# Kernel tuning notes

Hardware: AMD Instinct MI355X
Metric: run time of the kernel (lower is better)

Reference implementation:

```python
import jax, jax.numpy as jnp
import numpy as np

HID = 256
NUM_ENT = 100000
NUM_REL = 50
E = 320000  # edges per direction; edge_index has 2*E columns
BN_EPS = 1e-5


def setup_inputs() -> dict:
    key = jax.random.key(0)
    ks = jax.random.split(key, 10)
    x = jax.random.normal(ks[0], (NUM_ENT, HID), dtype=jnp.float32)
    edge_index = jax.random.randint(ks[1], (2, 2 * E), 0, NUM_ENT)
    edge_type = jax.random.randint(ks[2], (2 * E,), 0, NUM_REL)
    rel_embed = jax.random.normal(ks[3], (NUM_REL, HID), dtype=jnp.float32)
    # xavier_normal init: std = sqrt(2 / (fan_in + fan_out))
    w_std = (2.0 / (HID + HID)) ** 0.5
    w_loop = jax.random.normal(ks[4], (HID, HID), dtype=jnp.float32) * w_std
    w_in = jax.random.normal(ks[5], (HID, HID), dtype=jnp.float32) * w_std
    w_out = jax.random.normal(ks[6], (HID, HID), dtype=jnp.float32) * w_std
    w_rel = jax.random.normal(ks[7], (HID, HID), dtype=jnp.float32) * w_std
    loop_rel = jax.random.normal(ks[8], (1, HID), dtype=jnp.float32) * ((2.0 / (1 + HID)) ** 0.5)
    bn_weight = jnp.ones((HID,), dtype=jnp.float32)
    bn_bias = jnp.zeros((HID,), dtype=jnp.float32)
    return {
        "x": x, "edge_index": edge_index, "edge_type": edge_type,
        "rel_embed": rel_embed, "w_loop": w_loop, "w_in": w_in,
        "w_out": w_out, "w_rel": w_rel, "loop_rel": loop_rel,
        "bn_weight": bn_weight, "bn_bias": bn_bias,
    }


def _compute_norm(edge_index, num_ent):
    # symmetric D^-1/2 * D^-1/2 norm; degree counted on row (target) index
    row, col = edge_index[0], edge_index[1]
    deg = jax.ops.segment_sum(jnp.ones_like(row, dtype=jnp.float32), row, num_segments=num_ent)
    deg_inv = jnp.where(deg > 0, deg ** -0.5, 0.0)
    return deg_inv[row] * deg_inv[col]


def _propagate(x, idx, etype, rel_all, W, norm, num_ent):
    # gather source nodes (idx[1]), compose with relation emb (mult), transform, scale, scatter-add to targets (idx[0])
    msg = (x[idx[1]] * rel_all[etype]) @ W  # [E, d]
    if norm is not None:
        msg = msg * norm[:, None]
    return jax.ops.segment_sum(msg, idx[0], num_segments=num_ent)


def reference(x, edge_index, edge_type, rel_embed, w_loop, w_in, w_out, w_rel,
              loop_rel, bn_weight, bn_bias):
    num_ent = x.shape[0]
    rel_all = jnp.concatenate([rel_embed, loop_rel], axis=0)  # [R+1, d]
    e = edge_index.shape[1] // 2
    in_index, out_index = edge_index[:, :e], edge_index[:, e:]
    in_type, out_type = edge_type[:e], edge_type[e:]

    in_norm = _compute_norm(in_index, num_ent)
    out_norm = _compute_norm(out_index, num_ent)

    in_res = _propagate(x, in_index, in_type, rel_all, w_in, in_norm, num_ent)
    out_res = _propagate(x, out_index, out_type, rel_all, w_out, out_norm, num_ent)
    # self-loop: identity scatter -> just per-node compose+transform
    loop_res = (x * loop_rel) @ w_loop

    out = (in_res + out_res + loop_res) * (1.0 / 3.0)

    # BatchNorm1d in training mode (batch stats, biased variance)
    mean = out.mean(axis=0)
    var = out.var(axis=0)
    out = (out - mean) * jax.lax.rsqrt(var + BN_EPS) * bn_weight + bn_bias

    rel_out = (rel_all @ w_rel)[:-1]  # drop loop relation
    return out, rel_out
```

## Files before the change

### kernel.cpp

```cpp
#include <hip/hip_runtime.h>

#define HID     256
#define N_ENT   100000
#define TOT_E   640000
#define HALF_E  320000
#define NSEG    (2 * N_ENT)
#define BN_EPSF 1e-5f
#define SCAN_ELEMS 1024
#define NBLK_SCAN  ((NSEG + SCAN_ELEMS - 1) / SCAN_ELEMS)

typedef short bf16x8 __attribute__((ext_vector_type(8)));
typedef short bf16x4 __attribute__((ext_vector_type(4)));
typedef float f32x4  __attribute__((ext_vector_type(4)));

__device__ __forceinline__ short f2b(float f) {
    union { float f; unsigned u; } c; c.f = f;
    unsigned u = c.u;
    u += 0x7FFF + ((u >> 16) & 1);
    return (short)(u >> 16);
}
__device__ __forceinline__ float b2f(short b) {
    union { unsigned u; float f; } c;
    c.u = ((unsigned)(unsigned short)b) << 16;
    return c.f;
}

__global__ void hist_kernel(const int* __restrict__ ei, int* __restrict__ offs) {
    int j = blockIdx.x * 256 + threadIdx.x;
    if (j >= TOT_E) return;
    int seg = ei[j] + ((j < HALF_E) ? 0 : N_ENT);
    atomicAdd(&offs[seg], 1);
}

__global__ __launch_bounds__(256) void scan1(int* __restrict__ offs, int* __restrict__ bsums,
                                             float* __restrict__ rnorm) {
    __shared__ int tsum[256];
    int b = blockIdx.x, t = threadIdx.x;
    int base = b * SCAN_ELEMS + t * 4;
    int v[4] = {0, 0, 0, 0};
    if (base + 3 < NSEG) {
        int4 lv = *(const int4*)(offs + base);
        v[0] = lv.x; v[1] = lv.y; v[2] = lv.z; v[3] = lv.w;
    } else {
        for (int i = 0; i < 4; ++i) if (base + i < NSEG) v[i] = offs[base + i];
    }
    #pragma unroll
    for (int i = 0; i < 4; ++i)
        if (base + i < NSEG)
            rnorm[base + i] = (v[i] > 0) ? rsqrtf((float)v[i]) : 0.f;
    tsum[t] = v[0] + v[1] + v[2] + v[3];
    __syncthreads();
    for (int d = 1; d < 256; d <<= 1) {
        int val = (t >= d) ? tsum[t - d] : 0;
        __syncthreads();
        tsum[t] += val;
        __syncthreads();
    }
    int run = (t == 0) ? 0 : tsum[t - 1];
    if (t == 255) bsums[b] = tsum[255];
    int w[4];
    for (int i = 0; i < 4; ++i) { w[i] = run; run += v[i]; }
    if (base + 3 < NSEG) *(int4*)(offs + base) = make_int4(w[0], w[1], w[2], w[3]);
    else for (int i = 0; i < 4; ++i) if (base + i < NSEG) offs[base + i] = w[i];
}

__global__ __launch_bounds__(256) void scan3f(int* __restrict__ offs, const int* __restrict__ bsums) {
    __shared__ int tmp[256];
    int b = blockIdx.x, t = threadIdx.x;
    tmp[t] = (t < NBLK_SCAN) ? bsums[t] : 0;
    __syncthreads();
    for (int d = 1; d < 256; d <<= 1) {
        int val = (t >= d) ? tmp[t - d] : 0;
        __syncthreads();
        tmp[t] += val;
        __syncthreads();
    }
    int add = (b == 0) ? 0 : tmp[b - 1];
    int base = b * SCAN_ELEMS + t * 4;
    if (base + 3 < NSEG) {
        int4 v = *(int4*)(offs + base);
        v.x += add; v.y += add; v.z += add; v.w += add;
        *(int4*)(offs + base) = v;
    } else {
        for (int i = 0; i < 4; ++i) if (base + i < NSEG) offs[base + i] += add;
    }
}

__global__ void fill8_kernel(const int* __restrict__ ei, const int* __restrict__ et,
                             int* __restrict__ offs, const float* __restrict__ rnorm,
                             int2* __restrict__ elist8) {
    int j = blockIdx.x * 256 + threadIdx.x;
    if (j >= TOT_E) return;
    int hb  = (j < HALF_E) ? 0 : N_ENT;
    int seg = ei[j] + hb;
    int col = ei[TOT_E + j];
    float norm = rnorm[seg] * rnorm[hb + col];
    int pos = atomicAdd(&offs[seg], 1);
    elist8[pos] = make_int2(col | (et[j] << 17), __float_as_int(norm));
}

#define NX8 (N_ENT * HID / 8)
#define NR8 (50 * HID / 8)
__global__ void tobf16_both(const float* __restrict__ x, short* __restrict__ xh,
                            const float* __restrict__ rel, short* __restrict__ relh) {
    int i = blockIdx.x * 256 + threadIdx.x;
    const float* src; short* dst; int idx;
    if (i < NX8) { src = x; dst = xh; idx = i; }
    else if (i < NX8 + NR8) { src = rel; dst = relh; idx = i - NX8; }
    else return;
    const float4* p = (const float4*)(src + (size_t)idx * 8);
    float4 v0 = p[0], v1 = p[1];
    bf16x8 pk;
    pk[0]=f2b(v0.x); pk[1]=f2b(v0.y); pk[2]=f2b(v0.z); pk[3]=f2b(v0.w);
    pk[4]=f2b(v1.x); pk[5]=f2b(v1.y); pk[6]=f2b(v1.z); pk[7]=f2b(v1.w);
    *(bf16x8*)(dst + (size_t)idx * 8) = pk;
}

__global__ __launch_bounds__(256) void gather_h(
        const short* __restrict__ xh, const short* __restrict__ relh,
        const int* __restrict__ offs, const int2* __restrict__ elist8,
        short* __restrict__ accA, short* __restrict__ accB) {
    int s = blockIdx.x * 4 + (threadIdx.x >> 6);
    int lane = threadIdx.x & 63;
    int start = (s == 0) ? 0 : offs[s - 1];
    int end   = offs[s];
    float ax0=0.f, ay0=0.f, az0=0.f, aw0=0.f;
    float ax1=0.f, ay1=0.f, az1=0.f, aw1=0.f;
    int e = start;
    for (; e + 2 <= end; e += 2) {
        int2 p0 = elist8[e];
        int2 p1 = elist8[e + 1];
        int   c0 = p0.x & 0x1FFFF, t0 = p0.x >> 17;
        float n0 = __int_as_float(p0.y);
        int   c1 = p1.x & 0x1FFFF, t1 = p1.x >> 17;
        float n1 = __int_as_float(p1.y);
        bf16x4 xv0 = *(const bf16x4*)(xh   + (size_t)c0 * HID + lane * 4);
        bf16x4 rv0 = *(const bf16x4*)(relh + (size_t)t0 * HID + lane * 4);
        bf16x4 xv1 = *(const bf16x4*)(xh   + (size_t)c1 * HID + lane * 4);
        bf16x4 rv1 = *(const bf16x4*)(relh + (size_t)t1 * HID + lane * 4);
        ax0 += b2f(xv0[0]) * b2f(rv0[0]) * n0;
        ay0 += b2f(xv0[1]) * b2f(rv0[1]) * n0;
        az0 += b2f(xv0[2]) * b2f(rv0[2]) * n0;
        aw0 += b2f(xv0[3]) * b2f(rv0[3]) * n0;
        ax1 += b2f(xv1[0]) * b2f(rv1[0]) * n1;
        ay1 += b2f(xv1[1]) * b2f(rv1[1]) * n1;
        az1 += b2f(xv1[2]) * b2f(rv1[2]) * n1;
        aw1 += b2f(xv1[3]) * b2f(rv1[3]) * n1;
    }
    if (e < end) {
        int2 p = elist8[e];
        int   c = p.x & 0x1FFFF, t = p.x >> 17;
        float n = __int_as_float(p.y);
        bf16x4 xv = *(const bf16x4*)(xh   + (size_t)c * HID + lane * 4);
        bf16x4 rv = *(const bf16x4*)(relh + (size_t)t * HID + lane * 4);
        ax0 += b2f(xv[0]) * b2f(rv[0]) * n;
        ay0 += b2f(xv[1]) * b2f(rv[1]) * n;
        az0 += b2f(xv[2]) * b2f(rv[2]) * n;
        aw0 += b2f(xv[3]) * b2f(rv[3]) * n;
    }
    int hb = (s >= N_ENT) ? N_ENT : 0;
    short* dst = ((s >= N_ENT) ? accB : accA) + (size_t)(s - hb) * HID + lane * 4;
    bf16x4 pk;
    pk[0] = f2b(ax0 + ax1); pk[1] = f2b(ay0 + ay1);
    pk[2] = f2b(az0 + az1); pk[3] = f2b(aw0 + aw1);
    *(bf16x4*)dst = pk;
}

__global__ void wcat_kernel(const float* __restrict__ w_in, const float* __restrict__ w_out,
                            const float* __restrict__ w_loop, const float* __restrict__ loop_rel,
                            short* __restrict__ WT) {
    int n = blockIdx.x;
    int t = threadIdx.x;
    float v0 = w_in  [(size_t)t * HID + n];
    float v1 = w_out [(size_t)t * HID + n];
    float v2 = w_loop[(size_t)t * HID + n] * loop_rel[t];
    short* row = WT + (size_t)n * 768;
    row[t]       = f2b(v0);
    row[256 + t] = f2b(v1);
    row[512 + t] = f2b(v2);
}

template <bool BF16OUT>
__global__ __launch_bounds__(256, 2) void gemm_mfma_128(
        const short* __restrict__ accA, const short* __restrict__ accB,
        const short* __restrict__ xh, const short* __restrict__ WT,
        float* __restrict__ out, short* __restrict__ outh, float* __restrict__ stats)
{
    __shared__ __align__(16) short As[128 * 64];
    __shared__ __align__(16) short Bs[256 * 64];
    const int tid = threadIdx.x;
    const int l   = tid & 63;
    const int wid = tid >> 6;
    const int r0  = blockIdx.x * 128;
    const int lr  = l & 15;
    const int lg  = l >> 4;

    f32x4 acc[8][4];
    #pragma unroll
    for (int i = 0; i < 8; ++i)
        #pragma unroll
        for (int j = 0; j < 4; ++j)
            acc[i][j] = (f32x4){0.f, 0.f, 0.f, 0.f};

    const int sg = tid & 7;
    const int sr = tid >> 3;

    for (int kt = 0; kt < 12; ++kt) {
        const int src = kt >> 2;
        const short* Ap = (src == 0) ? accA : ((src == 1) ? accB : xh);
        const int ksg = kt * 64;
        const int ksl = (kt & 3) * 64;
        __syncthreads();
        #pragma unroll
        for (int h = 0; h < 4; ++h) {
            int r  = sr + 32 * h;
            int gr = r0 + r;
            bf16x8 v = {0,0,0,0,0,0,0,0};
            if (gr < N_ENT) v = *(const bf16x8*)(Ap + (size_t)gr * HID + ksl + sg * 8);
            *(bf16x8*)&As[r * 64 + ((sg ^ (r & 7)) << 3)] = v;
        }
        #pragma unroll
        for (int i = 0; i < 8; ++i) {
            int n = sr + 32 * i;
            bf16x8 w = *(const bf16x8*)(WT + (size_t)n * 768 + ksg + sg * 8);
            *(bf16x8*)&Bs[n * 64 + ((sg ^ (n & 7)) << 3)] = w;
        }
        __syncthreads();
        #pragma unroll
        for (int kc = 0; kc < 2; ++kc) {
            const int gsel = kc * 4 + lg;
            bf16x8 bfr[4];
            #pragma unroll
            for (int j = 0; j < 4; ++j) {
                int n = wid * 64 + 16 * j + lr;
                bfr[j] = *(const bf16x8*)&Bs[n * 64 + ((gsel ^ (n & 7)) << 3)];
            }
            #pragma unroll
            for (int i = 0; i < 8; ++i) {
                int r = 16 * i + lr;
                bf16x8 af = *(const bf16x8*)&As[r * 64 + ((gsel ^ (r & 7)) << 3)];
                #pragma unroll
                for (int j = 0; j < 4; ++j)
                    acc[i][j] = __builtin_amdgcn_mfma_f32_16x16x32_bf16(
                                    af, bfr[j], acc[i][j], 0, 0, 0);
            }
        }
    }

    const float third = 1.f / 3.f;
    float s[4]  = {0.f, 0.f, 0.f, 0.f};
    float sq[4] = {0.f, 0.f, 0.f, 0.f};
    #pragma unroll
    for (int i = 0; i < 8; ++i) {
        #pragma unroll
        for (int v = 0; v < 4; ++v) {
            int grow = r0 + 16 * i + lg * 4 + v;
            if (grow < N_ENT) {
                #pragma unroll
                for (int j = 0; j < 4; ++j) {
                    float val = acc[i][j][v] * third;
                    int col = wid * 64 + 16 * j + lr;
                    if (BF16OUT) outh[(size_t)grow * HID + col] = f2b(val);
                    else         out [(size_t)grow * HID + col] = val;
                    s[j] += val; sq[j] += val * val;
                }
            }
        }
    }
    #pragma unroll
    for (int j = 0; j < 4; ++j) {
        s[j]  += __shfl_xor(s[j], 16);  s[j]  += __shfl_xor(s[j], 32);
        sq[j] += __shfl_xor(sq[j], 16); sq[j] += __shfl_xor(sq[j], 32);
    }
    if (lg == 0) {
        #pragma unroll
        for (int j = 0; j < 4; ++j) {
            int c = wid * 64 + 16 * j + lr;
            atomicAdd(&stats[c], s[j]);
            atomicAdd(&stats[HID + c], sq[j]);
        }
    }
}

__global__ void bn_apply_h(const short* __restrict__ outh, float* __restrict__ out,
                           const float* __restrict__ stats,
                           const float* __restrict__ bnw, const float* __restrict__ bnb) {
    const float invN = 1.f / (float)N_ENT;
    const int total8 = N_ENT * (HID / 8);
    for (int i = blockIdx.x * 256 + threadIdx.x; i < total8; i += gridDim.x * 256) {
        int c = (i & 31) * 8;
        bf16x8 v = *(const bf16x8*)(outh + (size_t)i * 8);
        float r[8];
        #pragma unroll
        for (int k = 0; k < 8; ++k) {
            float mean = stats[c + k] * invN;
            float var  = stats[HID + c + k] * invN - mean * mean;
            float sc   = rsqrtf(var + BN_EPSF) * bnw[c + k];
            float sh   = bnb[c + k] - mean * sc;
            r[k] = b2f(v[k]) * sc + sh;
        }
        float4* dst = (float4*)(out + (size_t)i * 8);
        dst[0] = make_float4(r[0], r[1], r[2], r[3]);
        dst[1] = make_float4(r[4], r[5], r[6], r[7]);
    }
}

__global__ void bn_apply(float* __restrict__ out, const float* __restrict__ stats,
                         const float* __restrict__ bnw, const float* __restrict__ bnb) {
    const float invN = 1.f / (float)N_ENT;
    const int total4 = N_ENT * (HID / 4);
    for (int i = blockIdx.x * 256 + threadIdx.x; i < total4; i += gridDim.x * 256) {
        int c = (i & 63) * 4;
        float4 v = *(float4*)(out + (size_t)i * 4);
        #pragma unroll
        for (int k = 0; k < 4; ++k) {
            float mean = stats[c + k] * invN;
            float var  = stats[HID + c + k] * invN - mean * mean;
            float sc   = rsqrtf(var + BN_EPSF) * bnw[c + k];
            float sh   = bnb[c + k] - mean * sc;
            float* comp = (k == 0) ? &v.x : (k == 1) ? &v.y : (k == 2) ? &v.z : &v.w;
            *comp = (*comp) * sc + sh;
        }
        *(float4*)(out + (size_t)i * 4) = v;
    }
}

__global__ void relout_kernel(const float* __restrict__ rel_embed,
                              const float* __restrict__ w_rel,
                              float* __restrict__ rel_out) {
    __shared__ float row[HID];
    int r = blockIdx.x;
    int c = threadIdx.x;
    row[c] = rel_embed[(size_t)r * HID + c];
    __syncthreads();
    float s = 0.f;
    #pragma unroll 8
    for (int k = 0; k < HID; ++k) s += row[k] * w_rel[(size_t)k * HID + c];
    rel_out[(size_t)r * HID + c] = s;
}

extern "C" void kernel_launch(void* const* d_in, const int* in_sizes, int n_in,
                              void* d_out, int out_size, void* d_ws, size_t ws_size,
                              hipStream_t stream) {
    const float* x        = (const float*)d_in[0];
    const int*   ei       = (const int*)d_in[1];
    const int*   et       = (const int*)d_in[2];
    const float* rel      = (const float*)d_in[3];
    const float* w_loop   = (const float*)d_in[4];
    const float* w_in     = (const float*)d_in[5];
    const float* w_out    = (const float*)d_in[6];
    const float* w_rel    = (const float*)d_in[7];
    const float* loop_rel = (const float*)d_in[8];
    const float* bnw      = (const float*)d_in[9];
    const float* bnb      = (const float*)d_in[10];

    float* out     = (float*)d_out;
    float* rel_out = out + (size_t)N_ENT * HID;

    const size_t XH_B   = (size_t)N_ENT * HID * 2;
    const size_t ACC_B  = (size_t)N_ENT * HID * 2;
    const size_t OFFS_B = (size_t)NSEG * 4;
    const size_t EL8_B  = (size_t)TOT_E * 8;
    const size_t RN_B   = (size_t)NSEG * 4;
    const size_t RELH_B = (size_t)50 * HID * 2;
    const size_t base_need = XH_B + 2 * ACC_B + OFFS_B + EL8_B + RN_B
                           + 256 * 4 + 512 * 4 + RELH_B;
    const size_t OUTH_B = (size_t)N_ENT * HID * 2;
    const bool   have_outh = (ws_size >= base_need + OUTH_B);

    char* w = (char*)d_ws;
    short* xh     = (short*)w;              w += XH_B;
    short* accA_h = (short*)w;              w += ACC_B;
    short* accB_h = (short*)w;              w += ACC_B;
    int*   offs   = (int*)w;                w += OFFS_B;
    int2*  elist8 = (int2*)w;               short* WT = (short*)w;   w += EL8_B;
    float* rnorm  = (float*)w;              w += RN_B;
    int*   bsums  = (int*)w;                w += 256 * 4;
    float* stats  = (float*)w;              w += 512 * 4;
    short* relh   = (short*)w;              w += RELH_B;
    short* outh   = (short*)w;

    hipMemsetAsync(offs, 0, OFFS_B, stream);
    hipMemsetAsync(stats, 0, 512 * 4, stream);

    tobf16_both<<<(NX8 + NR8 + 255) / 256, 256, 0, stream>>>(x, xh, rel, relh);
    hist_kernel<<<TOT_E / 256, 256, 0, stream>>>(ei, offs);
    scan1<<<NBLK_SCAN, 256, 0, stream>>>(offs, bsums, rnorm);
    scan3f<<<NBLK_SCAN, 256, 0, stream>>>(offs, bsums);
    fill8_kernel<<<TOT_E / 256, 256, 0, stream>>>(ei, et, offs, rnorm, elist8);
    gather_h<<<NSEG / 4, 256, 0, stream>>>(xh, relh, offs, elist8, accA_h, accB_h);
    wcat_kernel<<<256, 256, 0, stream>>>(w_in, w_out, w_loop, loop_rel, WT);
    if (have_outh) {
        gemm_mfma_128<true><<<(N_ENT + 127) / 128, 256, 0, stream>>>(
            accA_h, accB_h, xh, WT, out, outh, stats);
        bn_apply_h<<<1024, 256, 0, stream>>>(outh, out, stats, bnw, bnb);
    } else {
        gemm_mfma_128<false><<<(N_ENT + 127) / 128, 256, 0, stream>>>(
            accA_h, accB_h, xh, WT, out, outh, stats);
        bn_apply<<<1024, 256, 0, stream>>>(out, stats, bnw, bnb);
    }
    relout_kernel<<<50, 256, 0, stream>>>(rel, w_rel, rel_out);
}
```

Before: 321.7 us.

## Load GEMM fragments directly from global and fuse small prep/epilogue kernels

Replaces the LDS-staged MFMA GEMM with a version where each wave loads bf16 fragments straight from global memory into registers and computes a 64x128 tile, removing shared-memory staging and barriers. It also merges the memsets, bf16 conversion and weight concat into one prep kernel, and folds the relation projection into the BN apply kernel, to cut launch overhead. WT gets a dedicated workspace slot. Risks: strided, poorly coalesced global fragment loads and heavier reliance on caches for reuse.

```diff
diff --git a/kernel.cpp b/kernel.cpp
--- a/kernel.cpp
+++ b/kernel.cpp
@@ -23,6 +23,44 @@
     union { unsigned u; float f; } c;
     c.u = ((unsigned)(unsigned short)b) << 16;
     return c.f;
+}
+
+#define NX8 (N_ENT * HID / 8)
+#define NR8 (50 * HID / 8)
+#define CONV_BLOCKS ((NX8 + NR8 + 255) / 256)
+__global__ void prep_kernel(const float* __restrict__ x, short* __restrict__ xh,
+                            const float* __restrict__ rel, short* __restrict__ relh,
+                            const float* __restrict__ w_in, const float* __restrict__ w_out,
+                            const float* __restrict__ w_loop, const float* __restrict__ loop_rel,
+                            short* __restrict__ WT,
+                            int* __restrict__ offs, float* __restrict__ stats) {
+    int bid = blockIdx.x;
+    int tid = threadIdx.x;
+    if (bid < CONV_BLOCKS) {
+        int i = bid * 256 + tid;
+        if (i < NSEG) offs[i] = 0;
+        if (i < 512) stats[i] = 0.f;
+        const float* src; short* dst; int idx;
+        if (i < NX8) { src = x; dst = xh; idx = i; }
+        else if (i < NX8 + NR8) { src = rel; dst = relh; idx = i - NX8; }
+        else return;
+        const float4* p = (const float4*)(src + (size_t)idx * 8);
+        float4 v0 = p[0], v1 = p[1];
+        bf16x8 pk;
+        pk[0]=f2b(v0.x); pk[1]=f2b(v0.y); pk[2]=f2b(v0.z); pk[3]=f2b(v0.w);
+        pk[4]=f2b(v1.x); pk[5]=f2b(v1.y); pk[6]=f2b(v1.z); pk[7]=f2b(v1.w);
+        *(bf16x8*)(dst + (size_t)idx * 8) = pk;
+    } else {
+        int n = bid - CONV_BLOCKS;
+        int t = tid;
+        float v0 = w_in  [(size_t)t * HID + n];
+        float v1 = w_out [(size_t)t * HID + n];
+        float v2 = w_loop[(size_t)t * HID + n] * loop_rel[t];
+        short* row = WT + (size_t)n * 768;
+        row[t]       = f2b(v0);
+        row[256 + t] = f2b(v1);
+        row[512 + t] = f2b(v2);
+    }
 }
 
 __global__ void hist_kernel(const int* __restrict__ ei, int* __restrict__ offs) {
@@ -97,23 +135,6 @@
     float norm = rnorm[seg] * rnorm[hb + col];
     int pos = atomicAdd(&offs[seg], 1);
     elist8[pos] = make_int2(col | (et[j] << 17), __float_as_int(norm));
-}
-
-#define NX8 (N_ENT * HID / 8)
-#define NR8 (50 * HID / 8)
-__global__ void tobf16_both(const float* __restrict__ x, short* __restrict__ xh,
-                            const float* __restrict__ rel, short* __restrict__ relh) {
-    int i = blockIdx.x * 256 + threadIdx.x;
-    const float* src; short* dst; int idx;
-    if (i < NX8) { src = x; dst = xh; idx = i; }
-    else if (i < NX8 + NR8) { src = rel; dst = relh; idx = i - NX8; }
-    else return;
-    const float4* p = (const float4*)(src + (size_t)idx * 8);
-    float4 v0 = p[0], v1 = p[1];
-    bf16x8 pk;
-    pk[0]=f2b(v0.x); pk[1]=f2b(v0.y); pk[2]=f2b(v0.z); pk[3]=f2b(v0.w);
-    pk[4]=f2b(v1.x); pk[5]=f2b(v1.y); pk[6]=f2b(v1.z); pk[7]=f2b(v1.w);
-    *(bf16x8*)(dst + (size_t)idx * 8) = pk;
 }
 
 __global__ __launch_bounds__(256) void gather_h(
@@ -166,100 +187,79 @@
     *(bf16x4*)dst = pk;
 }
 
-__global__ void wcat_kernel(const float* __restrict__ w_in, const float* __restrict__ w_out,
-                            const float* __restrict__ w_loop, const float* __restrict__ loop_rel,
-                            short* __restrict__ WT) {
-    int n = blockIdx.x;
-    int t = threadIdx.x;
-    float v0 = w_in  [(size_t)t * HID + n];
-    float v1 = w_out [(size_t)t * HID + n];
-    float v2 = w_loop[(size_t)t * HID + n] * loop_rel[t];
-    short* row = WT + (size_t)n * 768;
-    row[t]       = f2b(v0);
-    row[256 + t] = f2b(v1);
-    row[512 + t] = f2b(v2);
-}
-
 template <bool BF16OUT>
-__global__ __launch_bounds__(256, 2) void gemm_mfma_128(
+__global__ __launch_bounds__(256) void gemm_direct(
         const short* __restrict__ accA, const short* __restrict__ accB,
         const short* __restrict__ xh, const short* __restrict__ WT,
         float* __restrict__ out, short* __restrict__ outh, float* __restrict__ stats)
 {
-    __shared__ __align__(16) short As[128 * 64];
-    __shared__ __align__(16) short Bs[256 * 64];
     const int tid = threadIdx.x;
     const int l   = tid & 63;
     const int wid = tid >> 6;
-    const int r0  = blockIdx.x * 128;
+    const int wr  = wid >> 1;
+    const int wc  = wid & 1;
+    const int r0  = blockIdx.x * 128 + wr * 64;
+    const int c0  = wc * 128;
     const int lr  = l & 15;
     const int lg  = l >> 4;
-
-    f32x4 acc[8][4];
-    #pragma unroll
-    for (int i = 0; i < 8; ++i)
+    const int lgo = lg * 8;
+
+    f32x4 acc[4][8];
+    #pragma unroll
+    for (int i = 0; i < 4; ++i)
         #pragma unroll
-        for (int j = 0; j < 4; ++j)
+        for (int j = 0; j < 8; ++j)
             acc[i][j] = (f32x4){0.f, 0.f, 0.f, 0.f};
 
-    const int sg = tid & 7;
-    const int sr = tid >> 3;
-
-    for (int kt = 0; kt < 12; ++kt) {
-        const int src = kt >> 2;
-        const short* Ap = (src == 0) ? accA : ((src == 1) ? accB : xh);
-        const int ksg = kt * 64;
-        const int ksl = (kt & 3) * 64;
-        __syncthreads();
-        #pragma unroll
-        for (int h = 0; h < 4; ++h) {
-            int r  = sr + 32 * h;
-            int gr = r0 + r;
-            bf16x8 v = {0,0,0,0,0,0,0,0};
-            if (gr < N_ENT) v = *(const bf16x8*)(Ap + (size_t)gr * HID + ksl + sg * 8);
-            *(bf16x8*)&As[r * 64 + ((sg ^ (r & 7)) << 3)] = v;
+    int rowoff[4];
+    #pragma unroll
+    for (int i = 0; i < 4; ++i) {
+        int gr = r0 + 16 * i + lr;
+        if (gr >= N_ENT) gr = N_ENT - 1;
+        rowoff[i] = gr * HID;
+    }
+    int coloff[8];
+    #pragma unroll
+    for (int j = 0; j < 8; ++j)
+        coloff[j] = (c0 + 16 * j + lr) * 768;
+
+    #pragma unroll 1
+    for (int src = 0; src < 3; ++src) {
+        const short* __restrict__ Ap = (src == 0) ? accA : ((src == 1) ? accB : xh);
+        #pragma unroll 2
+        for (int c8 = 0; c8 < 8; ++c8) {
+            const int ka = c8 * 32 + lgo;
+            const int kb = src * 256 + c8 * 32 + lgo;
+            bf16x8 af[4], bfr[8];
+            #pragma unroll
+            for (int i = 0; i < 4; ++i)
+                af[i] = *(const bf16x8*)(Ap + (size_t)(rowoff[i] + ka));
+            #pragma unroll
+            for (int j = 0; j < 8; ++j)
+                bfr[j] = *(const bf16x8*)(WT + (size_t)(coloff[j] + kb));
+            #pragma unroll
+            for (int j = 0; j < 8; ++j)
+                #pragma unroll
+                for (int i = 0; i < 4; ++i)
+                    acc[i][j] = __builtin_amdgcn_mfma_f32_16x16x32_bf16(
+                                    af[i], bfr[j], acc[i][j], 0, 0, 0);
         }
-        #pragma unroll
-        for (int i = 0; i < 8; ++i) {
-            int n = sr + 32 * i;
-            bf16x8 w = *(const bf16x8*)(WT + (size_t)n * 768 + ksg + sg * 8);
-            *(bf16x8*)&Bs[n * 64 + ((sg ^ (n & 7)) << 3)] = w;
-        }
-        __syncthreads();
-        #pragma unroll
-        for (int kc = 0; kc < 2; ++kc) {
-            const int gsel = kc * 4 + lg;
-            bf16x8 bfr[4];
-            #pragma unroll
-            for (int j = 0; j < 4; ++j) {
-                int n = wid * 64 + 16 * j + lr;
-                bfr[j] = *(const bf16x8*)&Bs[n * 64 + ((gsel ^ (n & 7)) << 3)];
-            }
-            #pragma unroll
-            for (int i = 0; i < 8; ++i) {
-                int r = 16 * i + lr;
-                bf16x8 af = *(const bf16x8*)&As[r * 64 + ((gsel ^ (r & 7)) << 3)];
-                #pragma unroll
-                for (int j = 0; j < 4; ++j)
-                    acc[i][j] = __builtin_amdgcn_mfma_f32_16x16x32_bf16(
-                                    af, bfr[j], acc[i][j], 0, 0, 0);
-            }
-        }
     }
 
     const float third = 1.f / 3.f;
-    float s[4]  = {0.f, 0.f, 0.f, 0.f};
-    float sq[4] = {0.f, 0.f, 0.f, 0.f};
-    #pragma unroll
-    for (int i = 0; i < 8; ++i) {
+    float s[8], sq[8];
+    #pragma unroll
+    for (int j = 0; j < 8; ++j) { s[j] = 0.f; sq[j] = 0.f; }
+    #pragma unroll
+    for (int i = 0; i < 4; ++i) {
         #pragma unroll
         for (int v = 0; v < 4; ++v) {
             int grow = r0 + 16 * i + lg * 4 + v;
             if (grow < N_ENT) {
                 #pragma unroll
-                for (int j = 0; j < 4; ++j) {
+                for (int j = 0; j < 8; ++j) {
                     float val = acc[i][j][v] * third;
-                    int col = wid * 64 + 16 * j + lr;
+                    int col = c0 + 16 * j + lr;
                     if (BF16OUT) outh[(size_t)grow * HID + col] = f2b(val);
                     else         out [(size_t)grow * HID + col] = val;
                     s[j] += val; sq[j] += val * val;
@@ -268,75 +268,90 @@
         }
     }
     #pragma unroll
-    for (int j = 0; j < 4; ++j) {
+    for (int j = 0; j < 8; ++j) {
         s[j]  += __shfl_xor(s[j], 16);  s[j]  += __shfl_xor(s[j], 32);
         sq[j] += __shfl_xor(sq[j], 16); sq[j] += __shfl_xor(sq[j], 32);
     }
     if (lg == 0) {
         #pragma unroll
-        for (int j = 0; j < 4; ++j) {
-            int c = wid * 64 + 16 * j + lr;
+        for (int j = 0; j < 8; ++j) {
+            int c = c0 + 16 * j + lr;
             atomicAdd(&stats[c], s[j]);
             atomicAdd(&stats[HID + c], sq[j]);
         }
     }
 }
 
-__global__ void bn_apply_h(const short* __restrict__ outh, float* __restrict__ out,
-                           const float* __restrict__ stats,
-                           const float* __restrict__ bnw, const float* __restrict__ bnb) {
-    const float invN = 1.f / (float)N_ENT;
-    const int total8 = N_ENT * (HID / 8);
-    for (int i = blockIdx.x * 256 + threadIdx.x; i < total8; i += gridDim.x * 256) {
-        int c = (i & 31) * 8;
-        bf16x8 v = *(const bf16x8*)(outh + (size_t)i * 8);
-        float r[8];
-        #pragma unroll
-        for (int k = 0; k < 8; ++k) {
-            float mean = stats[c + k] * invN;
-            float var  = stats[HID + c + k] * invN - mean * mean;
-            float sc   = rsqrtf(var + BN_EPSF) * bnw[c + k];
-            float sh   = bnb[c + k] - mean * sc;
-            r[k] = b2f(v[k]) * sc + sh;
+#define BN_BLOCKS 1024
+__global__ void bn_relout_h(const short* __restrict__ outh, float* __restrict__ out,
+                            const float* __restrict__ stats,
+                            const float* __restrict__ bnw, const float* __restrict__ bnb,
+                            const float* __restrict__ rel_embed, const float* __restrict__ w_rel,
+                            float* __restrict__ rel_out) {
+    if (blockIdx.x < BN_BLOCKS) {
+        const float invN = 1.f / (float)N_ENT;
+        const int total8 = N_ENT * (HID / 8);
+        for (int i = blockIdx.x * 256 + threadIdx.x; i < total8; i += BN_BLOCKS * 256) {
+            int c = (i & 31) * 8;
+            bf16x8 v = *(const bf16x8*)(outh + (size_t)i * 8);
+            float r[8];
+            #pragma unroll
+            for (int k = 0; k < 8; ++k) {
+                float mean = stats[c + k] * invN;
+                float var  = stats[HID + c + k] * invN - mean * mean;
+                float sc   = rsqrtf(var + BN_EPSF) * bnw[c + k];
+                float sh   = bnb[c + k] - mean * sc;
+                r[k] = b2f(v[k]) * sc + sh;
+            }
+            float4* dst = (float4*)(out + (size_t)i * 8);
+            dst[0] = make_float4(r[0], r[1], r[2], r[3]);
+            dst[1] = make_float4(r[4], r[5], r[6], r[7]);
         }
-        float4* dst = (float4*)(out + (size_t)i * 8);
-        dst[0] = make_float4(r[0], r[1], r[2], r[3]);
-        dst[1] = make_float4(r[4], r[5], r[6], r[7]);
-    }
-}
-
-__global__ void bn_apply(float* __restrict__ out, const float* __restrict__ stats,
-                         const float* __restrict__ bnw, const float* __restrict__ bnb) {
-    const float invN = 1.f / (float)N_ENT;
-    const int total4 = N_ENT * (HID / 4);
-    for (int i = blockIdx.x * 256 + threadIdx.x; i < total4; i += gridDim.x * 256) {
-        int c = (i & 63) * 4;
-        float4 v = *(float4*)(out + (size_t)i * 4);
-        #pragma unroll
-        for (int k = 0; k < 4; ++k) {
-            float mean = stats[c + k] * invN;
-            float var  = stats[HID + c + k] * invN - mean * mean;
-            float sc   = rsqrtf(var + BN_EPSF) * bnw[c + k];
-            float sh   = bnb[c + k] - mean * sc;
-            float* comp = (k == 0) ? &v.x : (k == 1) ? &v.y : (k == 2) ? &v.z : &v.w;
-            *comp = (*comp) * sc + sh;
+    } else {
+        __shared__ float row[HID];
+        int r = blockIdx.x - BN_BLOCKS;
+        int c = threadIdx.x;
+        row[c] = rel_embed[(size_t)r * HID + c];
+        __syncthreads();
+        float sum = 0.f;
+        #pragma unroll 8
+        for (int k = 0; k < HID; ++k) sum += row[k] * w_rel[(size_t)k * HID + c];
+        rel_out[(size_t)r * HID + c] = sum;
+    }
+}
+
+__global__ void bn_relout_f(float* __restrict__ out, const float* __restrict__ stats,
+                            const float* __restrict__ bnw, const float* __restrict__ bnb,
+                            const float* __restrict__ rel_embed, const float* __restrict__ w_rel,
+                            float* __restrict__ rel_out) {
+    if (blockIdx.x < BN_BLOCKS) {
+        const float invN = 1.f / (float)N_ENT;
+        const int total4 = N_ENT * (HID / 4);
+        for (int i = blockIdx.x * 256 + threadIdx.x; i < total4; i += BN_BLOCKS * 256) {
+            int c = (i & 63) * 4;
+            float4 v = *(float4*)(out + (size_t)i * 4);
+            #pragma unroll
+            for (int k = 0; k < 4; ++k) {
+                float mean = stats[c + k] * invN;
+                float var  = stats[HID + c + k] * invN - mean * mean;
+                float sc   = rsqrtf(var + BN_EPSF) * bnw[c + k];
+                float sh   = bnb[c + k] - mean * sc;
+                float* comp = (k == 0) ? &v.x : (k == 1) ? &v.y : (k == 2) ? &v.z : &v.w;
+                *comp = (*comp) * sc + sh;
+            }
+            *(float4*)(out + (size_t)i * 4) = v;
         }
-        *(float4*)(out + (size_t)i * 4) = v;
-    }
-}
-
-__global__ void relout_kernel(const float* __restrict__ rel_embed,
-                              const float* __restrict__ w_rel,
-                              float* __restrict__ rel_out) {
-    __shared__ float row[HID];
-    int r = blockIdx.x;
-    int c = threadIdx.x;
-    row[c] = rel_embed[(size_t)r * HID + c];
-    __syncthreads();
-    float s = 0.f;
-    #pragma unroll 8
-    for (int k = 0; k < HID; ++k) s += row[k] * w_rel[(size_t)k * HID + c];
-    rel_out[(size_t)r * HID + c] = s;
+    } else {
+        __shared__ float row[HID];
+        int r = blockIdx.x - BN_BLOCKS;
+        int c = threadIdx.x;
+        row[c] = rel_embed[(size_t)r * HID + c];
+        __syncthreads();
+        float sum = 0.f;
+        #pragma unroll 8
+        for (int k = 0; k < HID; ++k) sum += row[k] * w_rel[(size_t)k * HID + c];
+        rel_out[(size_t)r * HID + c] = sum;
+    }
 }
 
 extern "C" void kernel_launch(void* const* d_in, const int* in_sizes, int n_in,
@@ -363,8 +378,9 @@
     const size_t EL8_B  = (size_t)TOT_E * 8;
     const size_t RN_B   = (size_t)NSEG * 4;
     const size_t RELH_B = (size_t)50 * HID * 2;
+    const size_t WT_B   = (size_t)256 * 768 * 2;
     const size_t base_need = XH_B + 2 * ACC_B + OFFS_B + EL8_B + RN_B
-                           + 256 * 4 + 512 * 4 + RELH_B;
+                           + 256 * 4 + 512 * 4 + RELH_B + WT_B;
     const size_t OUTH_B = (size_t)N_ENT * HID * 2;
     const bool   have_outh = (ws_size >= base_need + OUTH_B);
 
@@ -373,31 +389,31 @@
     short* accA_h = (short*)w;              w += ACC_B;
     short* accB_h = (short*)w;              w += ACC_B;
     int*   offs   = (int*)w;                w += OFFS_B;
-    int2*  elist8 = (int2*)w;               short* WT = (short*)w;   w += EL8_B;
+    int2*  elist8 = (int2*)w;               w += EL8_B;
     float* rnorm  = (float*)w;              w += RN_B;
     int*   bsums  = (int*)w;                w += 256 * 4;
     float* stats  = (float*)w;              w += 512 * 4;
     short* relh   = (short*)w;              w += RELH_B;
+    short* WT     = (short*)w;              w += WT_B;
     short* outh   = (short*)w;
 
-    hipMemsetAsync(offs, 0, OFFS_B, stream);
-    hipMemsetAsync(stats, 0, 512 * 4, stream);
-
-    tobf16_both<<<(NX8 + NR8 + 255) / 256, 256, 0, stream>>>(x, xh, rel, relh);
+    prep_kernel<<<CONV_BLOCKS + 256, 256, 0, stream>>>(x, xh, rel, relh,
+                                                       w_in, w_out, w_loop, loop_rel,
+                                                       WT, offs, stats);
     hist_kernel<<<TOT_E / 256, 256, 0, stream>>>(ei, offs);
     scan1<<<NBLK_SCAN, 256, 0, stream>>>(offs, bsums, rnorm);
     scan3f<<<NBLK_SCAN, 256, 0, stream>>>(offs, bsums);
     fill8_kernel<<<TOT_E / 256, 256, 0, stream>>>(ei, et, offs, rnorm, elist8);
     gather_h<<<NSEG / 4, 256, 0, stream>>>(xh, relh, offs, elist8, accA_h, accB_h);
-    wcat_kernel<<<256, 256, 0, stream>>>(w_in, w_out, w_loop, loop_rel, WT);
     if (have_outh) {
-        gemm_mfma_128<true><<<(N_ENT + 127) / 128, 256, 0, stream>>>(
+        gemm_direct<true><<<(N_ENT + 127) / 128, 256, 0, stream>>>(
             accA_h, accB_h, xh, WT, out, outh, stats);
-        bn_apply_h<<<1024, 256, 0, stream>>>(outh, out, stats, bnw, bnb);
-    } else {
-        gemm_mfma_128<false><<<(N_ENT + 127) / 128, 256, 0, stream>>>(
+        bn_relout_h<<<BN_BLOCKS + 50, 256, 0, stream>>>(outh, out, stats, bnw, bnb,
+                                                        rel, w_rel, rel_out);
+    } else {
+        gemm_direct<false><<<(N_ENT + 127) / 128, 256, 0, stream>>>(
             accA_h, accB_h, xh, WT, out, outh, stats);
-        bn_apply<<<1024, 256, 0, stream>>>(out, stats, bnw, bnb);
-    }
-    relout_kernel<<<50, 256, 0, stream>>>(rel, w_rel, rel_out);
-}
+        bn_relout_f<<<BN_BLOCKS + 50, 256, 0, stream>>>(out, stats, bnw, bnb,
+                                                        rel, w_rel, rel_out);
+    }
+}
```

New measurement: 385.9 us. 20.0% more time.
